# Kernel optimization log

Measured on AMD Instinct MI355X. Metric: run time of the kernel, lower is better.

Reference implementation:

```python
import jax, jax.numpy as jnp
import numpy as np
from jax import lax

_S = 0.7071067811865476
_LO = np.array([_S, _S], np.float32)   # pywt haar dec_lo[::-1] == rec_lo
_HI = np.array([_S, -_S], np.float32)  # pywt haar dec_hi[::-1] == rec_hi

def _outer(a, b):
    # torch: a.unsqueeze(0) * b.unsqueeze(1)  -> w[i, j] = a[j] * b[i]
    return a[None, :] * b[:, None]

# subband filters in order ll, lh, hl, hh; identical for dec and rec with haar
_FILT = jnp.asarray(np.stack([_outer(_LO, _LO), _outer(_LO, _HI), _outer(_HI, _LO), _outer(_HI, _HI)]))  # (4,2,2)


def conv1x1(x, w, b=None):
    y = jnp.einsum('bchw,oc->bohw', x, w)
    return y if b is None else y + b[None, :, None, None]


def dwt_haar(x):
    # depthwise stride-2 2x2 conv per subband, concat [ll,lh,hl,hh] along channels
    B, C, H, W = x.shape
    xr = x.reshape(B, C, H // 2, 2, W // 2, 2)
    sub = jnp.einsum('bchdwe,sde->bschw', xr, _FILT)  # (B,4,C,H/2,W/2)
    return sub.reshape(B, 4 * C, H // 2, W // 2)


def idwt_haar(x):
    # stride-2 2x2 transposed conv: non-overlapping -> exact block interleave
    B, C4, H, W = x.shape
    C = C4 // 4
    xs = x.reshape(B, 4, C, H, W)
    y = jnp.einsum('bschw,sde->bchdwe', xs, _FILT)  # (B,C,H,2,W,2)
    return y.reshape(B, C, 2 * H, 2 * W)


def idynamic(out, x_dwt, w1, b1, w2, b2, K=7):
    # kernel-generating branch from x_dwt, depthwise-grouped dynamic KxK conv on out
    B, C, H, W = out.shape
    G = w2.shape[0] // (K * K)
    gc = C // G
    t = jax.nn.relu(conv1x1(x_dwt, w1, b1))
    wgen = conv1x1(t, w2, b2).reshape(B, G, K * K, H, W)
    pad = K // 2
    xp = jnp.pad(out.reshape(B, G, gc, H, W), ((0, 0), (0, 0), (0, 0), (pad, pad), (pad, pad)))
    acc = jnp.zeros((B, G, gc, H, W), out.dtype)
    for di in range(K):
        for dj in range(K):
            acc = acc + xp[:, :, :, di:di + H, dj:dj + W] * wgen[:, :, di * K + dj][:, :, None]
    return acc.reshape(B, C, H, W)


def setup_inputs() -> dict:
    key = jax.random.key(0)
    ks = jax.random.split(key, 9)
    B, dim, H, W = 2, 128, 256, 256
    heads, K = 8, 7
    G = dim // heads  # group_channels=num_heads -> groups = dim // num_heads
    return {
        'x': jax.random.normal(ks[0], (B, dim, H, W), jnp.float32),
        'reduce_w': jax.random.normal(ks[1], (dim // 4, dim), jnp.float32) * 0.05,
        'reduce_b': jnp.zeros((dim // 4,), jnp.float32),
        'qkv_w': jax.random.normal(ks[2], (dim * 3, dim), jnp.float32) * 0.05,
        'qkv_dw': jax.random.normal(ks[3], (dim * 3, 1, 3, 3), jnp.float32) * 0.1,
        'temperature': jnp.ones((heads, 1, 1), jnp.float32),
        'fil_w1': jax.random.normal(ks[4], (dim // 4, dim), jnp.float32) * 0.05,
        'fil_b1': jnp.zeros((dim // 4,), jnp.float32),
        'fil_w2': jax.random.normal(ks[5], (G * K * K, dim // 4), jnp.float32) * 0.05,
        'fil_b2': jnp.zeros((G * K * K,), jnp.float32),
        'proj_w': jax.random.normal(ks[6], (dim, dim // 4), jnp.float32) * 0.05,
    }


def reference(x, reduce_w, reduce_b, qkv_w, qkv_dw, temperature, fil_w1, fil_b1, fil_w2, fil_b2, proj_w):
    num_heads = temperature.shape[0]
    B, dim, H, W = x.shape
    # reduce + DWT: dim -> dim//4 -> dim channels at half resolution
    r = jax.nn.relu(conv1x1(x, reduce_w, reduce_b))
    x_dwt = dwt_haar(r)  # (B, dim, H/2, W/2)
    # QKV pointwise + depthwise 3x3
    qkv = conv1x1(x_dwt, qkv_w)
    qkv = lax.conv_general_dilated(qkv, qkv_dw, (1, 1), ((1, 1), (1, 1)),
                                   feature_group_count=dim * 3,
                                   dimension_numbers=('NCHW', 'OIHW', 'NCHW'))
    h2, w2 = H // 2, W // 2
    c = dim // num_heads
    q, k, v = jnp.split(qkv, 3, axis=1)
    q = q.reshape(B, num_heads, c, h2 * w2)
    k = k.reshape(B, num_heads, c, h2 * w2)
    v = v.reshape(B, num_heads, c, h2 * w2)
    # L2 normalize over spatial axis (F.normalize eps=1e-12)
    q = q / jnp.clip(jnp.linalg.norm(q, axis=-1, keepdims=True), 1e-12)
    k = k / jnp.clip(jnp.linalg.norm(k, axis=-1, keepdims=True), 1e-12)
    attn = jnp.einsum('bhcn,bhdn->bhcd', q, k) * temperature[None]
    attn = jax.nn.relu(attn)  # activation='relu'
    out = jnp.einsum('bhcd,bhdn->bhcn', attn, v).reshape(B, dim, h2, w2)
    out = idynamic(out, x_dwt, fil_w1, fil_b1, fil_w2, fil_b2)
    out = idwt_haar(out)            # (B, dim//4, H, W)
    out = conv1x1(out, proj_w)      # (B, dim, H, W)
    return out
```

## Files before the change

kernel.cpp:

```cpp
#include <hip/hip_runtime.h>
#include <math.h>

#define BB 2
#define DIM 128
#define HH 256
#define WW 256
#define HWFULL 65536
#define HHW 16384
#define HEADS 8
#define CHEAD 16
#define KK 7
#define GG 16
#define GC 8
#define NCHUNK 8

__global__ __launch_bounds__(128) void k_reduce_dwt(
        const float* __restrict__ x, const float* __restrict__ w,
        const float* __restrict__ bias, float* __restrict__ xd) {
    int p   = blockIdx.x * 128 + threadIdx.x;
    int oc0 = blockIdx.y * 8;
    int b   = blockIdx.z;
    int hq = p >> 7, wq = p & 127;

    __shared__ __align__(16) float wl[128 * 8];
    for (int i = threadIdx.x; i < 128 * 8; i += 128) {
        int oc = i & 7, c = i >> 3;
        wl[i] = w[(size_t)(oc0 + oc) * 128 + c];
    }
    __syncthreads();

    float accA[8], accB[8], accC[8], accD[8];
#pragma unroll
    for (int oc = 0; oc < 8; oc++) {
        float bv = bias[oc0 + oc];
        accA[oc] = bv; accB[oc] = bv; accC[oc] = bv; accD[oc] = bv;
    }

    const float* xb = x + (size_t)b * 128 * HWFULL;
    int rowT = (2 * hq) * 256 + 2 * wq;
    int rowB = rowT + 256;
#pragma unroll 4
    for (int c = 0; c < 128; c++) {
        float2 top = *reinterpret_cast<const float2*>(&xb[(size_t)c * HWFULL + rowT]);
        float2 bot = *reinterpret_cast<const float2*>(&xb[(size_t)c * HWFULL + rowB]);
        const float4* wc = reinterpret_cast<const float4*>(&wl[c * 8]);
        float4 w40 = wc[0], w41 = wc[1];
        float wv[8] = {w40.x, w40.y, w40.z, w40.w, w41.x, w41.y, w41.z, w41.w};
#pragma unroll
        for (int oc = 0; oc < 8; oc++) {
            accA[oc] = fmaf(top.x, wv[oc], accA[oc]);
            accB[oc] = fmaf(top.y, wv[oc], accB[oc]);
            accC[oc] = fmaf(bot.x, wv[oc], accC[oc]);
            accD[oc] = fmaf(bot.y, wv[oc], accD[oc]);
        }
    }

    float* xbase = xd + (size_t)b * 128 * HHW + p;
#pragma unroll
    for (int oc = 0; oc < 8; oc++) {
        float a = fmaxf(accA[oc], 0.f);
        float bq = fmaxf(accB[oc], 0.f);
        float c2 = fmaxf(accC[oc], 0.f);
        float d = fmaxf(accD[oc], 0.f);
        int ch = oc0 + oc;
        xbase[(size_t)(0 * 32 + ch) * HHW] = 0.5f * (a + bq + c2 + d);
        xbase[(size_t)(1 * 32 + ch) * HHW] = 0.5f * (a + bq - c2 - d);
        xbase[(size_t)(2 * 32 + ch) * HHW] = 0.5f * (a - bq + c2 - d);
        xbase[(size_t)(3 * 32 + ch) * HHW] = 0.5f * (a - bq - c2 + d);
    }
}

template<int PX, int OCB, int IC>
__global__ __launch_bounds__(256) void k_conv1x1(
        const float* __restrict__ x, const float* __restrict__ w,
        const float* __restrict__ bias, float* __restrict__ y,
        int OC, int P, int do_relu) {
    int p0  = blockIdx.x * (256 * PX) + threadIdx.x;
    int oc0 = blockIdx.y * OCB;
    int b   = blockIdx.z;

    __shared__ __align__(16) float wl[IC * OCB];
    for (int i = threadIdx.x; i < IC * OCB; i += 256) {
        int oc = i & (OCB - 1), c = i / OCB;
        wl[i] = w[(size_t)(oc0 + oc) * IC + c];
    }
    __syncthreads();

    float acc[PX][OCB];
#pragma unroll
    for (int px = 0; px < PX; px++)
#pragma unroll
        for (int oc = 0; oc < OCB; oc++) acc[px][oc] = bias ? bias[oc0 + oc] : 0.f;

    const float* xb = x + (size_t)b * IC * P;
#pragma unroll 4
    for (int c = 0; c < IC; c++) {
        float xv[PX];
#pragma unroll
        for (int px = 0; px < PX; px++) xv[px] = xb[(size_t)c * P + p0 + px * 256];
        const float4* wc = reinterpret_cast<const float4*>(&wl[c * OCB]);
#pragma unroll
        for (int q = 0; q < OCB / 4; q++) {
            float4 w4 = wc[q];
#pragma unroll
            for (int px = 0; px < PX; px++) {
                acc[px][4*q+0] = fmaf(xv[px], w4.x, acc[px][4*q+0]);
                acc[px][4*q+1] = fmaf(xv[px], w4.y, acc[px][4*q+1]);
                acc[px][4*q+2] = fmaf(xv[px], w4.z, acc[px][4*q+2]);
                acc[px][4*q+3] = fmaf(xv[px], w4.w, acc[px][4*q+3]);
            }
        }
    }
    float* yb = y + ((size_t)b * OC + oc0) * P;
#pragma unroll
    for (int oc = 0; oc < OCB; oc++)
#pragma unroll
        for (int px = 0; px < PX; px++) {
            float v = acc[px][oc];
            yb[(size_t)oc * P + p0 + px * 256] = do_relu ? fmaxf(v, 0.f) : v;
        }
}

#define DWR 32
__global__ __launch_bounds__(256) void k_dw3x3(const float* __restrict__ x,
                                               const float* __restrict__ w,
                                               float* __restrict__ y) {
    int blk = blockIdx.x;
    int rt = blk & 3;
    int ch = blk >> 2;
    int r0 = rt * DWR;

    __shared__ float tile[(DWR + 2) * 130];
    const float* xp = x + (size_t)ch * HHW;

    for (int i = threadIdx.x; i < (DWR + 2) * 130; i += 256) {
        int r = i / 130, c = i % 130;
        int gy = r0 + r - 1, gx = c - 1;
        float v = 0.f;
        if (gy >= 0 && gy < 128 && gx >= 0 && gx < 128)
            v = xp[gy * 128 + gx];
        tile[i] = v;
    }
    __syncthreads();

    const float* wc = w + (size_t)(ch % 384) * 9;
    float w00 = wc[0], w01 = wc[1], w02 = wc[2];
    float w10 = wc[3], w11 = wc[4], w12 = wc[5];
    float w20 = wc[6], w21 = wc[7], w22 = wc[8];

    int tx = threadIdx.x & 127;
    int ty = threadIdx.x >> 7;
    int lrbase = ty * 16;

    const float* lp = &tile[lrbase * 130 + tx];
    float t0 = lp[0], t1 = lp[1], t2 = lp[2];
    lp += 130;
    float m0 = lp[0], m1 = lp[1], m2 = lp[2];

    float* yp = y + (size_t)ch * HHW + (r0 + ty * 16) * 128 + tx;
#pragma unroll
    for (int i = 0; i < 16; i++) {
        lp += 130;
        float b0 = lp[0], b1 = lp[1], b2 = lp[2];
        float a0 = t0 * w00 + t1 * w01 + t2 * w02;
        float a1 = m0 * w10 + m1 * w11 + m2 * w12;
        float a2 = b0 * w20 + b1 * w21 + b2 * w22;
        yp[i * 128] = a0 + a1 + a2;
        t0 = m0; t1 = m1; t2 = m2;
        m0 = b0; m1 = b1; m2 = b2;
    }
}

__global__ void k_norms(const float* __restrict__ qkv, float* __restrict__ norms) {
    int blk = blockIdx.x;
    int b = blk >> 8;
    int ch = blk & 255;
    const float* p = qkv + ((size_t)b * 384 + ch) * HHW;
    float s = 0.f;
    for (int i = threadIdx.x; i < HHW; i += 256) {
        float v = p[i];
        s = fmaf(v, v, s);
    }
#pragma unroll
    for (int off = 32; off > 0; off >>= 1) s += __shfl_down(s, off);
    __shared__ float red[4];
    int lane = threadIdx.x & 63, wid = threadIdx.x >> 6;
    if (lane == 0) red[wid] = s;
    __syncthreads();
    if (threadIdx.x == 0) {
        float t = red[0] + red[1] + red[2] + red[3];
        norms[b * 256 + ch] = fmaxf(sqrtf(t), 1e-12f);
    }
}

__global__ void k_attn_s(const float* __restrict__ qkv, float* __restrict__ Spart) {
    int blk = blockIdx.x;
    int chunk = blockIdx.y;
    int ci = blk & 15;
    int hd = (blk >> 4) & 7;
    int b  = blk >> 7;
    const float* q = qkv + ((size_t)b * 384 + hd * CHEAD + ci) * HHW;
    const float* k = qkv + ((size_t)b * 384 + 128 + hd * CHEAD) * HHW;

    float acc[16];
#pragma unroll
    for (int cj = 0; cj < 16; cj++) acc[cj] = 0.f;

    int n0 = chunk * (HHW / NCHUNK);
    int n1 = n0 + (HHW / NCHUNK);
    for (int n = n0 + threadIdx.x; n < n1; n += 256) {
        float qv = q[n];
#pragma unroll
        for (int cj = 0; cj < 16; cj++) acc[cj] = fmaf(qv, k[(size_t)cj * HHW + n], acc[cj]);
    }

    __shared__ float red[4][16];
    int lane = threadIdx.x & 63, wid = threadIdx.x >> 6;
#pragma unroll
    for (int cj = 0; cj < 16; cj++) {
        float v = acc[cj];
#pragma unroll
        for (int off = 32; off > 0; off >>= 1) v += __shfl_down(v, off);
        if (lane == 0) red[wid][cj] = v;
    }
    __syncthreads();
    if (threadIdx.x < 16) {
        int cj = threadIdx.x;
        float s = red[0][cj] + red[1][cj] + red[2][cj] + red[3][cj];
        Spart[(size_t)chunk * 4096 + ((((size_t)b * 8 + hd) * 16 + ci) * 16 + cj)] = s;
    }
}

__global__ void k_attn_norm(const float* __restrict__ Spart, const float* __restrict__ norms,
                            const float* __restrict__ temp, float* __restrict__ attn) {
    int i = blockIdx.x * 256 + threadIdx.x;
    if (i >= BB * 8 * 16 * 16) return;
    int cj = i & 15, ci = (i >> 4) & 15, hd = (i >> 8) & 7, b = i >> 11;
    float s = 0.f;
#pragma unroll
    for (int ch = 0; ch < NCHUNK; ch++) s += Spart[(size_t)ch * 4096 + i];
    float qn = norms[b * 256 + hd * CHEAD + ci];
    float kn = norms[b * 256 + 128 + hd * CHEAD + cj];
    attn[i] = fmaxf(s / (qn * kn) * temp[hd], 0.f);
}

__global__ void k_attn_apply(const float* __restrict__ qkv, const float* __restrict__ attn,
                             float* __restrict__ out) {
    int n = blockIdx.x * 256 + threadIdx.x;
    int hd = blockIdx.y;
    int b = blockIdx.z;

    __shared__ float at[256];
    at[threadIdx.x] = attn[((size_t)b * 8 + hd) * 256 + threadIdx.x];
    __syncthreads();

    const float* v = qkv + ((size_t)b * 384 + 256 + hd * CHEAD) * HHW + n;
    float vv[16];
#pragma unroll
    for (int cj = 0; cj < 16; cj++) vv[cj] = v[(size_t)cj * HHW];

    float* ob = out + ((size_t)b * 128 + hd * CHEAD) * HHW + n;
#pragma unroll
    for (int ci = 0; ci < 16; ci++) {
        float acc = 0.f;
        const float* ar = &at[ci * 16];
#pragma unroll
        for (int cj = 0; cj < 16; cj++) acc = fmaf(ar[cj], vv[cj], acc);
        ob[(size_t)ci * HHW] = acc;
    }
}

__global__ void k_dyn(const float* __restrict__ oa, const float* __restrict__ t,
                      const float* __restrict__ w2, const float* __restrict__ b2,
                      float* __restrict__ od) {
    int tile = blockIdx.x;
    int g = blockIdx.y;
    int b = blockIdx.z;
    int ty0 = (tile >> 3) * 16, tx0 = (tile & 7) * 16;
    int ty = threadIdx.x >> 4, tx = threadIdx.x & 15;
    int y = ty0 + ty, x = tx0 + tx;

    __shared__ __align__(16) float patch[8][22][22];
    const float* oab = oa + ((size_t)b * 128 + g * GC) * HHW;
    for (int i = threadIdx.x; i < 8 * 22 * 22; i += 256) {
        int cc = i / 484;
        int rem = i % 484;
        int py = rem / 22, px = rem % 22;
        int sy = ty0 + py - 3, sx = tx0 + px - 3;
        float v = 0.f;
        if (sy >= 0 && sy < 128 && sx >= 0 && sx < 128)
            v = oab[(size_t)cc * HHW + sy * 128 + sx];
        patch[cc][py][px] = v;
    }
    __syncthreads();

    const float* tb = t + (size_t)b * 32 * HHW + y * 128 + x;
    float tv[32];
#pragma unroll
    for (int m = 0; m < 32; m++) tv[m] = tb[(size_t)m * HHW];

    const float* w2g = w2 + (size_t)g * 49 * 32;
    const float* b2g = b2 + (size_t)g * 49;

    float acc[8];
#pragma unroll
    for (int cc = 0; cc < 8; cc++) acc[cc] = 0.f;

    for (int kk = 0; kk < 49; kk++) {
        float w0 = b2g[kk], w1 = 0.f;
        const float* wr = &w2g[kk * 32];
#pragma unroll
        for (int m = 0; m < 32; m += 2) {
            w0 = fmaf(wr[m],     tv[m],     w0);
            w1 = fmaf(wr[m + 1], tv[m + 1], w1);
        }
        float wv = w0 + w1;
        int di = kk / 7, dj = kk % 7;
#pragma unroll
        for (int cc = 0; cc < 8; cc++)
            acc[cc] = fmaf(patch[cc][ty + di][tx + dj], wv, acc[cc]);
    }

    float* odb = od + ((size_t)b * 128 + g * GC) * HHW + y * 128 + x;
#pragma unroll
    for (int cc = 0; cc < 8; cc++) odb[(size_t)cc * HHW] = acc[cc];
}

__global__ void k_idwt_proj(const float* __restrict__ dyn, const float* __restrict__ pw,
                            float* __restrict__ out) {
    int p = blockIdx.x * 256 + threadIdx.x;
    int oc0 = blockIdx.y * 16;
    int b = blockIdx.z;
    int y = p >> 7, x = p & 127;

    __shared__ __align__(16) float wl[32 * 16];
    for (int i = threadIdx.x; i < 512; i += 256) {
        int oc = i & 15, c = i >> 4;
        wl[i] = pw[(size_t)(oc0 + oc) * 32 + c];
    }
    __syncthreads();

    float u0[16], u1[16], u2[16], u3[16];
#pragma unroll
    for (int oc = 0; oc < 16; oc++) { u0[oc]=0.f; u1[oc]=0.f; u2[oc]=0.f; u3[oc]=0.f; }

    const float* db = dyn + (size_t)b * 128 * HHW + p;
    for (int c = 0; c < 32; c++) {
        float d0 = db[(size_t)(0 * 32 + c) * HHW];
        float d1 = db[(size_t)(1 * 32 + c) * HHW];
        float d2 = db[(size_t)(2 * 32 + c) * HHW];
        float d3 = db[(size_t)(3 * 32 + c) * HHW];
        const float* wc = &wl[c * 16];
#pragma unroll
        for (int oc = 0; oc < 16; oc++) {
            float wv = wc[oc];
            u0[oc] = fmaf(wv, d0, u0[oc]);
            u1[oc] = fmaf(wv, d1, u1[oc]);
            u2[oc] = fmaf(wv, d2, u2[oc]);
            u3[oc] = fmaf(wv, d3, u3[oc]);
        }
    }

    float* ob = out + ((size_t)b * 128 + oc0) * HWFULL + (2 * y) * 256 + 2 * x;
#pragma unroll
    for (int oc = 0; oc < 16; oc++) {
        float a = u0[oc], bq = u1[oc], c2 = u2[oc], dd = u3[oc];
        float2 top, bot;
        top.x = 0.5f * (a + bq + c2 + dd);
        top.y = 0.5f * (a + bq - c2 - dd);
        bot.x = 0.5f * (a - bq + c2 - dd);
        bot.y = 0.5f * (a - bq - c2 + dd);
        float* o = ob + (size_t)oc * HWFULL;
        *reinterpret_cast<float2*>(&o[0])   = top;
        *reinterpret_cast<float2*>(&o[256]) = bot;
    }
}

extern "C" void kernel_launch(void* const* d_in, const int* in_sizes, int n_in,
                              void* d_out, int out_size, void* d_ws, size_t ws_size,
                              hipStream_t stream) {
    const float* x        = (const float*)d_in[0];
    const float* reduce_w = (const float*)d_in[1];
    const float* reduce_b = (const float*)d_in[2];
    const float* qkv_w    = (const float*)d_in[3];
    const float* qkv_dw   = (const float*)d_in[4];
    const float* temp     = (const float*)d_in[5];
    const float* fil_w1   = (const float*)d_in[6];
    const float* fil_b1   = (const float*)d_in[7];
    const float* fil_w2   = (const float*)d_in[8];
    const float* fil_b2   = (const float*)d_in[9];
    const float* proj_w   = (const float*)d_in[10];
    float* out = (float*)d_out;

    float* ws = (float*)d_ws;
    float* x_dwt = ws;
    float* big   = x_dwt + (size_t)BB * 128 * HHW;
    float* qkv1  = big   + (size_t)BB * 384 * HHW;
    float* tbuf  = qkv1  + (size_t)BB * 384 * HHW;
    float* norms = tbuf  + (size_t)BB * 32 * HHW;
    float* Spart = norms + 512;
    float* attn  = Spart + NCHUNK * 4096;
    float* qkv0 = big;
    float* out_attn = big;
    float* out_dyn = x_dwt;

    k_reduce_dwt<<<dim3(HHW / 128, 4, BB), 128, 0, stream>>>(x, reduce_w, reduce_b, x_dwt);
    k_conv1x1<2, 16, 128><<<dim3(HHW / 512, 384 / 16, BB), 256, 0, stream>>>(
        x_dwt, qkv_w, nullptr, qkv0, 384, HHW, 0);
    k_dw3x3<<<dim3(BB * 384 * 4), 256, 0, stream>>>(qkv0, qkv_dw, qkv1);
    k_norms<<<dim3(BB * 256), 256, 0, stream>>>(qkv1, norms);
    k_attn_s<<<dim3(BB * 8 * 16, NCHUNK), 256, 0, stream>>>(qkv1, Spart);
    k_attn_norm<<<dim3(16), 256, 0, stream>>>(Spart, norms, temp, attn);
    k_attn_apply<<<dim3(HHW / 256, HEADS, BB), 256, 0, stream>>>(qkv1, attn, out_attn);
    k_conv1x1<1, 16, 128><<<dim3(HHW / 256, 2, BB), 256, 0, stream>>>(
        x_dwt, fil_w1, fil_b1, tbuf, 32, HHW, 1);
    k_dyn<<<dim3(64, GG, BB), 256, 0, stream>>>(out_attn, tbuf, fil_w2, fil_b2, out_dyn);
    k_idwt_proj<<<dim3(HHW / 256, 8, BB), 256, 0, stream>>>(out_dyn, proj_w, out);
}
```

Before: 348.6 us.

## Restructure reduce+DWT per-pixel threads with shuffles; drop LDS weight staging in 1x1 convs

The reduce+DWT kernel now gives each thread one full-resolution pixel and all 32 output channels. The input is read only once instead of four times across channel blocks, and the Haar butterfly is done with warp xor-shuffles among the four quad threads. The 1x1 conv kernels stop staging weights in shared memory and read uniform weights straight from global, which lets the compiler use scalar loads. The QKV conv moves to a float4-per-thread variant, and the filter conv's output-channel block shrinks from 16 to 8. The tradeoffs are more registers per thread (32 accumulators), lane-strided non-vector input loads in the reduce kernel, and reliance on scalar cache for the weights.

Measured after the change: 376.0 us. 7.9% more time.

```diff
diff --git a/kernel.cpp b/kernel.cpp
--- a/kernel.cpp
+++ b/kernel.cpp
@@ -14,59 +14,77 @@
 #define GC 8
 #define NCHUNK 8
 
-__global__ __launch_bounds__(128) void k_reduce_dwt(
+__global__ __launch_bounds__(256) void k_reduce_dwt(
         const float* __restrict__ x, const float* __restrict__ w,
         const float* __restrict__ bias, float* __restrict__ xd) {
-    int p   = blockIdx.x * 128 + threadIdx.x;
-    int oc0 = blockIdx.y * 8;
-    int b   = blockIdx.z;
+    int t = threadIdx.x;
+    int pix = t >> 2, pos = t & 3;
+    int p = blockIdx.x * 64 + pix;
+    int b = blockIdx.y;
     int hq = p >> 7, wq = p & 127;
-
-    __shared__ __align__(16) float wl[128 * 8];
-    for (int i = threadIdx.x; i < 128 * 8; i += 128) {
-        int oc = i & 7, c = i >> 3;
-        wl[i] = w[(size_t)(oc0 + oc) * 128 + c];
-    }
-    __syncthreads();
-
-    float accA[8], accB[8], accC[8], accD[8];
-#pragma unroll
-    for (int oc = 0; oc < 8; oc++) {
-        float bv = bias[oc0 + oc];
-        accA[oc] = bv; accB[oc] = bv; accC[oc] = bv; accD[oc] = bv;
-    }
-
-    const float* xb = x + (size_t)b * 128 * HWFULL;
-    int rowT = (2 * hq) * 256 + 2 * wq;
-    int rowB = rowT + 256;
+    int gy = 2 * hq + (pos >> 1), gx = 2 * wq + (pos & 1);
+
+    float acc[32];
+#pragma unroll
+    for (int oc = 0; oc < 32; oc++) acc[oc] = bias[oc];
+
+    const float* xb = x + (size_t)b * 128 * HWFULL + gy * 256 + gx;
 #pragma unroll 4
     for (int c = 0; c < 128; c++) {
-        float2 top = *reinterpret_cast<const float2*>(&xb[(size_t)c * HWFULL + rowT]);
-        float2 bot = *reinterpret_cast<const float2*>(&xb[(size_t)c * HWFULL + rowB]);
-        const float4* wc = reinterpret_cast<const float4*>(&wl[c * 8]);
-        float4 w40 = wc[0], w41 = wc[1];
-        float wv[8] = {w40.x, w40.y, w40.z, w40.w, w41.x, w41.y, w41.z, w41.w};
-#pragma unroll
-        for (int oc = 0; oc < 8; oc++) {
-            accA[oc] = fmaf(top.x, wv[oc], accA[oc]);
-            accB[oc] = fmaf(top.y, wv[oc], accB[oc]);
-            accC[oc] = fmaf(bot.x, wv[oc], accC[oc]);
-            accD[oc] = fmaf(bot.y, wv[oc], accD[oc]);
+        float xv = xb[(size_t)c * HWFULL];
+#pragma unroll
+        for (int oc = 0; oc < 32; oc++)
+            acc[oc] = fmaf(xv, w[oc * 128 + c], acc[oc]);
+    }
+
+    float s1 = (pos & 1) ? -1.f : 1.f;
+    float s2 = (pos & 2) ? -1.f : 1.f;
+    int s = ((pos & 1) << 1) | (pos >> 1);
+    float* xo = xd + (size_t)b * 128 * HHW + (size_t)s * 32 * HHW + p;
+#pragma unroll
+    for (int oc = 0; oc < 32; oc++) {
+        float v = fmaxf(acc[oc], 0.f);
+        float t1 = __shfl_xor(v, 1);
+        float r1 = fmaf(s1, v, t1);
+        float t2 = __shfl_xor(r1, 2);
+        float r2 = fmaf(s2, r1, t2);
+        xo[(size_t)oc * HHW] = 0.5f * r2;
+    }
+}
+
+template<int OCB, int IC>
+__global__ __launch_bounds__(256) void k_conv1x1_f4(
+        const float* __restrict__ x, const float* __restrict__ w,
+        float* __restrict__ y, int OC, int P) {
+    int p0  = (blockIdx.x * 256 + threadIdx.x) * 4;
+    int oc0 = blockIdx.y * OCB;
+    int b   = blockIdx.z;
+
+    float acc[4][OCB];
+#pragma unroll
+    for (int px = 0; px < 4; px++)
+#pragma unroll
+        for (int oc = 0; oc < OCB; oc++) acc[px][oc] = 0.f;
+
+    const float* xb = x + (size_t)b * IC * P;
+    const float* wb = w + (size_t)oc0 * IC;
+#pragma unroll 4
+    for (int c = 0; c < IC; c++) {
+        float4 xv = *reinterpret_cast<const float4*>(&xb[(size_t)c * P + p0]);
+#pragma unroll
+        for (int oc = 0; oc < OCB; oc++) {
+            float wv = wb[oc * IC + c];
+            acc[0][oc] = fmaf(xv.x, wv, acc[0][oc]);
+            acc[1][oc] = fmaf(xv.y, wv, acc[1][oc]);
+            acc[2][oc] = fmaf(xv.z, wv, acc[2][oc]);
+            acc[3][oc] = fmaf(xv.w, wv, acc[3][oc]);
         }
     }
-
-    float* xbase = xd + (size_t)b * 128 * HHW + p;
-#pragma unroll
-    for (int oc = 0; oc < 8; oc++) {
-        float a = fmaxf(accA[oc], 0.f);
-        float bq = fmaxf(accB[oc], 0.f);
-        float c2 = fmaxf(accC[oc], 0.f);
-        float d = fmaxf(accD[oc], 0.f);
-        int ch = oc0 + oc;
-        xbase[(size_t)(0 * 32 + ch) * HHW] = 0.5f * (a + bq + c2 + d);
-        xbase[(size_t)(1 * 32 + ch) * HHW] = 0.5f * (a + bq - c2 - d);
-        xbase[(size_t)(2 * 32 + ch) * HHW] = 0.5f * (a - bq + c2 - d);
-        xbase[(size_t)(3 * 32 + ch) * HHW] = 0.5f * (a - bq - c2 + d);
+    float* yb = y + ((size_t)b * OC + oc0) * P;
+#pragma unroll
+    for (int oc = 0; oc < OCB; oc++) {
+        float4 o = make_float4(acc[0][oc], acc[1][oc], acc[2][oc], acc[3][oc]);
+        *reinterpret_cast<float4*>(&yb[(size_t)oc * P + p0]) = o;
     }
 }
 
@@ -79,13 +97,6 @@
     int oc0 = blockIdx.y * OCB;
     int b   = blockIdx.z;
 
-    __shared__ __align__(16) float wl[IC * OCB];
-    for (int i = threadIdx.x; i < IC * OCB; i += 256) {
-        int oc = i & (OCB - 1), c = i / OCB;
-        wl[i] = w[(size_t)(oc0 + oc) * IC + c];
-    }
-    __syncthreads();
-
     float acc[PX][OCB];
 #pragma unroll
     for (int px = 0; px < PX; px++)
@@ -93,22 +104,18 @@
         for (int oc = 0; oc < OCB; oc++) acc[px][oc] = bias ? bias[oc0 + oc] : 0.f;
 
     const float* xb = x + (size_t)b * IC * P;
+    const float* wb = w + (size_t)oc0 * IC;
 #pragma unroll 4
     for (int c = 0; c < IC; c++) {
         float xv[PX];
 #pragma unroll
         for (int px = 0; px < PX; px++) xv[px] = xb[(size_t)c * P + p0 + px * 256];
-        const float4* wc = reinterpret_cast<const float4*>(&wl[c * OCB]);
-#pragma unroll
-        for (int q = 0; q < OCB / 4; q++) {
-            float4 w4 = wc[q];
-#pragma unroll
-            for (int px = 0; px < PX; px++) {
-                acc[px][4*q+0] = fmaf(xv[px], w4.x, acc[px][4*q+0]);
-                acc[px][4*q+1] = fmaf(xv[px], w4.y, acc[px][4*q+1]);
-                acc[px][4*q+2] = fmaf(xv[px], w4.z, acc[px][4*q+2]);
-                acc[px][4*q+3] = fmaf(xv[px], w4.w, acc[px][4*q+3]);
-            }
+#pragma unroll
+        for (int oc = 0; oc < OCB; oc++) {
+            float wv = wb[oc * IC + c];
+#pragma unroll
+            for (int px = 0; px < PX; px++)
+                acc[px][oc] = fmaf(xv[px], wv, acc[px][oc]);
         }
     }
     float* yb = y + ((size_t)b * OC + oc0) * P;
@@ -404,15 +411,15 @@
     float* out_attn = big;
     float* out_dyn = x_dwt;
 
-    k_reduce_dwt<<<dim3(HHW / 128, 4, BB), 128, 0, stream>>>(x, reduce_w, reduce_b, x_dwt);
-    k_conv1x1<2, 16, 128><<<dim3(HHW / 512, 384 / 16, BB), 256, 0, stream>>>(
-        x_dwt, qkv_w, nullptr, qkv0, 384, HHW, 0);
+    k_reduce_dwt<<<dim3(HHW / 64, BB), 256, 0, stream>>>(x, reduce_w, reduce_b, x_dwt);
+    k_conv1x1_f4<16, 128><<<dim3(HHW / 1024, 384 / 16, BB), 256, 0, stream>>>(
+        x_dwt, qkv_w, qkv0, 384, HHW);
     k_dw3x3<<<dim3(BB * 384 * 4), 256, 0, stream>>>(qkv0, qkv_dw, qkv1);
     k_norms<<<dim3(BB * 256), 256, 0, stream>>>(qkv1, norms);
     k_attn_s<<<dim3(BB * 8 * 16, NCHUNK), 256, 0, stream>>>(qkv1, Spart);
     k_attn_norm<<<dim3(16), 256, 0, stream>>>(Spart, norms, temp, attn);
     k_attn_apply<<<dim3(HHW / 256, HEADS, BB), 256, 0, stream>>>(qkv1, attn, out_attn);
-    k_conv1x1<1, 16, 128><<<dim3(HHW / 256, 2, BB), 256, 0, stream>>>(
+    k_conv1x1<1, 8, 128><<<dim3(HHW / 256, 4, BB), 256, 0, stream>>>(
         x_dwt, fil_w1, fil_b1, tbuf, 32, HHW, 1);
     k_dyn<<<dim3(64, GG, BB), 256, 0, stream>>>(out_attn, tbuf, fil_w2, fil_b2, out_dyn);
     k_idwt_proj<<<dim3(HHW / 256, 8, BB), 256, 0, stream>>>(out_dyn, proj_w, out);
```
